# Optimization experiments

Hardware: AMD Instinct MI355X
Metric: run time of the kernel (lower is better)

The kernel has to match this reference:

```python
import jax, jax.numpy as jnp
import numpy as np

H = 256          # h_dim
SEQ_LEN = 10     # max history length
B = 2048         # number of queries with non-empty history
N = 327680       # total flattened neighbors across all (query, timestep) segments
NUM_SEG = B * SEQ_LEN
NUM_ENT = 20000
NUM_REL = 200


def setup_inputs() -> dict:
    key = jax.random.key(0)
    ks = jax.random.split(key, 9)
    s = jax.random.randint(ks[0], (B,), 0, NUM_ENT)
    r = jax.random.randint(ks[1], (B,), 0, NUM_REL)
    nbr_ids = jax.random.randint(ks[2], (N,), 0, NUM_ENT)
    seg_ids = jnp.sort(jax.random.randint(ks[3], (N,), 0, NUM_SEG))
    ent_embeds = jax.random.normal(ks[4], (NUM_ENT, H), dtype=jnp.float32)
    rel_embeds = jax.random.normal(ks[5], (NUM_REL, H), dtype=jnp.float32)
    W_attn = jax.random.normal(ks[6], (3 * H, H), dtype=jnp.float32) * 0.05
    b_attn = jax.random.normal(ks[7], (H,), dtype=jnp.float32) * 0.05
    v_s = jax.random.normal(ks[8], (H, 1), dtype=jnp.float32) * 0.05
    return {"s": s, "r": r, "nbr_ids": nbr_ids, "seg_ids": seg_ids,
            "ent_embeds": ent_embeds, "rel_embeds": rel_embeds,
            "W_attn": W_attn, "b_attn": b_attn, "v_s": v_s}


def reference(s, r, nbr_ids, seg_ids, ent_embeds, rel_embeds, W_attn, b_attn, v_s):
    # Per-neighbor gathers. Each neighbor belongs to segment seg = q*SEQ_LEN + t.
    q = seg_ids // SEQ_LEN                              # query index per neighbor [N]
    em = ent_embeds[nbr_ids]                            # [N, H] neighbor embeddings
    s_emb = ent_embeds[s]                               # [B, H]
    r_emb = rel_embeds[r]                               # [B, H]
    ss = s_emb[q]                                       # [N, H]
    rr = r_emb[q]                                       # [N, H]
    # Score: tanh(Linear(3H -> H)) @ v_s  -> scalar per neighbor
    x = jnp.concatenate([em, ss, rr], axis=1)           # [N, 3H]
    scores = (jnp.tanh(x @ W_attn + b_attn) @ v_s)[:, 0]  # [N]
    # Segment softmax over neighbors within each (query, timestep) segment.
    m = jax.ops.segment_max(scores, seg_ids, num_segments=NUM_SEG)  # [S]
    e = jnp.exp(scores - m[seg_ids])                    # [N]
    denom = jax.ops.segment_sum(e, seg_ids, num_segments=NUM_SEG)   # [S]
    w = e / denom[seg_ids]                              # [N]
    # Weighted sum of neighbor embeddings per segment (scatter-reduce).
    agg = jax.ops.segment_sum(w[:, None] * em, seg_ids, num_segments=NUM_SEG)  # [S, H]
    counts = jax.ops.segment_sum(jnp.ones_like(scores), seg_ids, num_segments=NUM_SEG)
    mask = (counts > 0).astype(em.dtype).reshape(B, SEQ_LEN, 1)     # present timesteps
    agg = agg.reshape(B, SEQ_LEN, H)
    ss_t = jnp.broadcast_to(s_emb[:, None, :], (B, SEQ_LEN, H))
    rr_t = jnp.broadcast_to(r_emb[:, None, :], (B, SEQ_LEN, H))
    # Padded [B, SEQ_LEN, 3H] sequence tensor (rows for empty segments are zero,
    # matching the torch code's zero-initialized padded tensor). Dropout p=0.0.
    out = jnp.concatenate([agg, ss_t, rr_t], axis=2) * mask
    return out
```

## Files before the change

### kernel.cpp

```cpp
#include <hip/hip_runtime.h>
#include <hip/hip_bf16.h>

#define H 256
#define SEQ 10
#define C2LOG2E 2.8853900817779268f
#define LOG2E 1.4426950408889634f

typedef __attribute__((ext_vector_type(8))) short bf16x8;
typedef __attribute__((ext_vector_type(4))) float f32x4;

__device__ __forceinline__ unsigned short f2bf(float x) {
    union { float f; unsigned u; } v; v.f = x;
    unsigned r = v.u + 0x7fff + ((v.u >> 16) & 1);
    return (unsigned short)(r >> 16);
}
__device__ __forceinline__ float bf2f(unsigned short b) {
    union { unsigned u; float f; } v; v.u = ((unsigned)b) << 16;
    return v.f;
}
__device__ __forceinline__ float fexp2(float x) {
    return __builtin_amdgcn_exp2f(x);
}

__global__ void prep_kernel(const float* __restrict__ W,
                            unsigned short* __restrict__ Wt,
                            const int* __restrict__ seg_ids,
                            int* __restrict__ seg_start,
                            int nTr, int n, int num_seg) {
    if ((int)blockIdx.x < nTr) {
        __shared__ float tile[64][65];
        int tk = blockIdx.x % 12;
        int tn = blockIdx.x / 12;
        int t = threadIdx.x;
        int rr = t >> 2;
        int rc = (t & 3) * 16;
        const float* src = W + (size_t)(tk * 64 + rr) * H + tn * 64 + rc;
        float4 a = *reinterpret_cast<const float4*>(src);
        float4 b = *reinterpret_cast<const float4*>(src + 4);
        float4 c = *reinterpret_cast<const float4*>(src + 8);
        float4 d = *reinterpret_cast<const float4*>(src + 12);
        tile[rr][rc + 0] = a.x;  tile[rr][rc + 1] = a.y;
        tile[rr][rc + 2] = a.z;  tile[rr][rc + 3] = a.w;
        tile[rr][rc + 4] = b.x;  tile[rr][rc + 5] = b.y;
        tile[rr][rc + 6] = b.z;  tile[rr][rc + 7] = b.w;
        tile[rr][rc + 8] = c.x;  tile[rr][rc + 9] = c.y;
        tile[rr][rc + 10] = c.z; tile[rr][rc + 11] = c.w;
        tile[rr][rc + 12] = d.x; tile[rr][rc + 13] = d.y;
        tile[rr][rc + 14] = d.z; tile[rr][rc + 15] = d.w;
        __syncthreads();
        bf16x8 o0, o1;
#pragma unroll
        for (int j = 0; j < 8; j++) {
            o0[j] = (short)f2bf(C2LOG2E * tile[rc + j][rr]);
            o1[j] = (short)f2bf(C2LOG2E * tile[rc + 8 + j][rr]);
        }
        unsigned short* dst = Wt + (size_t)(tn * 64 + rr) * (3 * H) + tk * 64 + rc;
        *reinterpret_cast<bf16x8*>(dst) = o0;
        *reinterpret_cast<bf16x8*>(dst + 8) = o1;
    } else {
        int j = (blockIdx.x - nTr) * 256 + threadIdx.x;
        if (j >= n) return;
        int cur = seg_ids[j];
        int prev = (j == 0) ? -1 : seg_ids[j - 1];
        for (int s2 = prev + 1; s2 <= cur; s2++) seg_start[s2] = j;
        if (j == n - 1)
            for (int s2 = cur + 1; s2 <= num_seg; s2++) seg_start[s2] = n;
    }
}

__global__ void gemm_bf16_kernel(const float* __restrict__ entf,
                                 const int* __restrict__ sidx,
                                 const int* __restrict__ ridx,
                                 const float* __restrict__ rel,
                                 const unsigned short* __restrict__ Wt,
                                 const float* __restrict__ bias,
                                 unsigned short* __restrict__ comb,
                                 unsigned short* __restrict__ qpart,
                                 int nEntBlk, int M0, int M1) {
    __shared__ unsigned short As[64][40];
    bool isEnt = (int)blockIdx.x < nEntBlk;
    int m0 = (isEnt ? blockIdx.x : (blockIdx.x - nEntBlk)) * 64;
    int M = isEnt ? M0 : M1;
    int K = isEnt ? H : 2 * H;
    int k0 = isEnt ? 0 : H;
    int ldo = isEnt ? 512 : H;
    unsigned short* outp = isEnt ? comb : qpart;

    int t = threadIdx.x;
    int sr = t >> 2;
    int sc = (t & 3) * 8;
    int wave = t >> 6, lane = t & 63;
    int lr = lane & 15, lg = lane >> 4;

    f32x4 acc[4][4];
#pragma unroll
    for (int i = 0; i < 4; i++)
#pragma unroll
        for (int jn = 0; jn < 4; jn++) acc[i][jn] = (f32x4){0.f, 0.f, 0.f, 0.f};

    const unsigned short* bp[4];
#pragma unroll
    for (int bn = 0; bn < 4; bn++)
        bp[bn] = Wt + (size_t)(wave * 64 + bn * 16 + lr) * (3 * H) + k0 + lg * 8;

    for (int kk = 0; kk < K; kk += 32) {
        bf16x8 av = {};
        int gm = m0 + sr;
        if (gm < M) {
            const float* src;
            if (isEnt) {
                src = entf + (size_t)gm * H + kk + sc;
            } else {
                int k = kk + sc;
                src = (k < H) ? (entf + (size_t)sidx[gm] * H + k)
                              : (rel + (size_t)ridx[gm] * H + (k - H));
            }
            float4 f0 = *reinterpret_cast<const float4*>(src);
            float4 f1 = *reinterpret_cast<const float4*>(src + 4);
            av[0] = (short)f2bf(f0.x); av[1] = (short)f2bf(f0.y);
            av[2] = (short)f2bf(f0.z); av[3] = (short)f2bf(f0.w);
            av[4] = (short)f2bf(f1.x); av[5] = (short)f2bf(f1.y);
            av[6] = (short)f2bf(f1.z); av[7] = (short)f2bf(f1.w);
            if (isEnt)
                *reinterpret_cast<bf16x8*>(comb + (size_t)gm * 512 + 256 + kk + sc) = av;
        }
        *reinterpret_cast<bf16x8*>(&As[sr][sc]) = av;

        bf16x8 bfr[4];
#pragma unroll
        for (int bn = 0; bn < 4; bn++)
            bfr[bn] = *reinterpret_cast<const bf16x8*>(bp[bn] + kk);

        __syncthreads();
        bf16x8 afr[4];
#pragma unroll
        for (int am = 0; am < 4; am++)
            afr[am] = *reinterpret_cast<const bf16x8*>(&As[am * 16 + lr][lg * 8]);
#pragma unroll
        for (int am = 0; am < 4; am++)
#pragma unroll
            for (int bn = 0; bn < 4; bn++)
                acc[am][bn] = __builtin_amdgcn_mfma_f32_16x16x32_bf16(
                    afr[am], bfr[bn], acc[am][bn], 0, 0, 0);
        __syncthreads();
    }

#pragma unroll
    for (int bn = 0; bn < 4; bn++) {
        int col = wave * 64 + bn * 16 + lr;
        float bv = isEnt ? 0.f : C2LOG2E * bias[col];
#pragma unroll
        for (int am = 0; am < 4; am++) {
#pragma unroll
            for (int rr = 0; rr < 4; rr++) {
                int row = m0 + am * 16 + lg * 4 + rr;
                if (row < M)
                    outp[(size_t)row * ldo + col] = f2bf(acc[am][bn][rr] + bv);
            }
        }
    }
}

__global__ void __launch_bounds__(128)
fused_agg_kernel(const int* __restrict__ nbr_ids,
                 const int* __restrict__ seg_start,
                 const unsigned short* __restrict__ comb,
                 const unsigned short* __restrict__ qpartbf,
                 const float* __restrict__ v_s,
                 const float* __restrict__ ent_embeds,
                 const float* __restrict__ rel_embeds,
                 const int* __restrict__ s,
                 const int* __restrict__ r,
                 float* __restrict__ out, int num_seg) {
    int seg = blockIdx.x * 2 + (threadIdx.x >> 6);
    if (seg >= num_seg) return;
    int lane = threadIdx.x & 63;
    int g = lane >> 4, li = lane & 15;
    int cb = li * 16;
    int c4 = lane * 4;
    int b = seg / SEQ;
    int start = seg_start[seg], end = seg_start[seg + 1];
    float* orow = out + (size_t)seg * (3 * H);

    if (start == end) {
        float4 z = {0.f, 0.f, 0.f, 0.f};
        *reinterpret_cast<float4*>(orow + c4) = z;
        *reinterpret_cast<float4*>(orow + H + c4) = z;
        *reinterpret_cast<float4*>(orow + 2 * H + c4) = z;
        return;
    }

    float4 ssv = *reinterpret_cast<const float4*>(ent_embeds + (size_t)s[b] * H + c4);
    float4 rrv = *reinterpret_cast<const float4*>(rel_embeds + (size_t)r[b] * H + c4);

    float vm2[16];
    float vsum = 0.f;
    {
        const float4* vp = reinterpret_cast<const float4*>(v_s + cb);
#pragma unroll
        for (int k = 0; k < 4; k++) {
            float4 tv = vp[k];
            vm2[4 * k + 0] = -2.f * tv.x; vm2[4 * k + 1] = -2.f * tv.y;
            vm2[4 * k + 2] = -2.f * tv.z; vm2[4 * k + 3] = -2.f * tv.w;
            vsum += tv.x + tv.y + tv.z + tv.w;
        }
    }

    float qv[16];
    {
        bf16x8 qa = *reinterpret_cast<const bf16x8*>(qpartbf + (size_t)b * H + cb);
        bf16x8 qb = *reinterpret_cast<const bf16x8*>(qpartbf + (size_t)b * H + cb + 8);
#pragma unroll
        for (int k = 0; k < 8; k++) {
            qv[k] = bf2f((unsigned short)qa[k]);
            qv[8 + k] = bf2f((unsigned short)qb[k]);
        }
    }

    float acc[16];
#pragma unroll
    for (int k = 0; k < 16; k++) acc[k] = 0.f;
    float lpart = 0.f;

    int cc = end - start;
    int nitm = (cc + 3) >> 2;

    bf16x8 p0 = {}, p1 = {}, e0 = {}, e1 = {};
    if (g < cc) {
        const unsigned short* row = comb + (size_t)nbr_ids[start + g] * 512 + cb;
        p0 = *reinterpret_cast<const bf16x8*>(row);
        p1 = *reinterpret_cast<const bf16x8*>(row + 8);
        e0 = *reinterpret_cast<const bf16x8*>(row + 256);
        e1 = *reinterpret_cast<const bf16x8*>(row + 264);
    }

    for (int ji = 0; ji < nitm; ji++) {
        bf16x8 p0n = {}, p1n = {}, e0n = {}, e1n = {};
        int jn = 4 * (ji + 1) + g;
        if (jn < cc) {
            const unsigned short* rown = comb + (size_t)nbr_ids[start + jn] * 512 + cb;
            p0n = *reinterpret_cast<const bf16x8*>(rown);
            p1n = *reinterpret_cast<const bf16x8*>(rown + 8);
            e0n = *reinterpret_cast<const bf16x8*>(rown + 256);
            e1n = *reinterpret_cast<const bf16x8*>(rown + 264);
        }

        float sa = 0.f, sb = 0.f;
#pragma unroll
        for (int k = 0; k < 8; k += 2) {
            float a0 = fexp2(bf2f((unsigned short)p0[k]) + qv[k]) + 1.f;
            float a1 = fexp2(bf2f((unsigned short)p1[k]) + qv[8 + k]) + 1.f;
            float num = vm2[k] * a1;
            num = fmaf(vm2[8 + k], a0, num);
            sa = fmaf(num, __builtin_amdgcn_rcpf(a0 * a1), sa);
            float b0 = fexp2(bf2f((unsigned short)p0[k + 1]) + qv[k + 1]) + 1.f;
            float b1 = fexp2(bf2f((unsigned short)p1[k + 1]) + qv[9 + k]) + 1.f;
            float numb = vm2[k + 1] * b1;
            numb = fmaf(vm2[9 + k], b0, numb);
            sb = fmaf(numb, __builtin_amdgcn_rcpf(b0 * b1), sb);
        }
        float s16 = sa + sb + vsum;
        s16 += __shfl_xor(s16, 1);
        s16 += __shfl_xor(s16, 2);
        s16 += __shfl_xor(s16, 4);
        s16 += __shfl_xor(s16, 8);
        float e = fexp2(s16 * LOG2E);
        e = (4 * ji + g < cc) ? e : 0.f;
        lpart += e;
#pragma unroll
        for (int k = 0; k < 8; k++) {
            acc[k] = fmaf(e, bf2f((unsigned short)e0[k]), acc[k]);
            acc[8 + k] = fmaf(e, bf2f((unsigned short)e1[k]), acc[8 + k]);
        }
        p0 = p0n; p1 = p1n; e0 = e0n; e1 = e1n;
    }

    lpart += __shfl_xor(lpart, 16);
    lpart += __shfl_xor(lpart, 32);
#pragma unroll
    for (int k = 0; k < 16; k++) {
        acc[k] += __shfl_xor(acc[k], 16);
        acc[k] += __shfl_xor(acc[k], 32);
    }
    float invl = 1.f / lpart;

    float4 o;
#pragma unroll
    for (int k = 0; k < 4; k++) {
        float v0 = acc[k], v1 = acc[4 + k], v2 = acc[8 + k], v3 = acc[12 + k];
        float pick = (g == 0) ? v0 : (g == 1) ? v1 : (g == 2) ? v2 : v3;
        if (k == 0) o.x = pick * invl;
        else if (k == 1) o.y = pick * invl;
        else if (k == 2) o.z = pick * invl;
        else o.w = pick * invl;
    }
    *reinterpret_cast<float4*>(orow + cb + 4 * g) = o;
    *reinterpret_cast<float4*>(orow + H + c4) = ssv;
    *reinterpret_cast<float4*>(orow + 2 * H + c4) = rrv;
}

extern "C" void kernel_launch(void* const* d_in, const int* in_sizes, int n_in,
                              void* d_out, int out_size, void* d_ws, size_t ws_size,
                              hipStream_t stream) {
    const int* s = (const int*)d_in[0];
    const int* r = (const int*)d_in[1];
    const int* nbr_ids = (const int*)d_in[2];
    const int* seg_ids = (const int*)d_in[3];
    const float* ent_embeds = (const float*)d_in[4];
    const float* rel_embeds = (const float*)d_in[5];
    const float* W_attn = (const float*)d_in[6];
    const float* b_attn = (const float*)d_in[7];
    const float* v_s = (const float*)d_in[8];
    float* out = (float*)d_out;

    int B = in_sizes[0];
    int N = in_sizes[2];
    int num_ent = in_sizes[4] / H;
    int num_seg = B * SEQ;

    char* ws = (char*)d_ws;
    unsigned short* comb = (unsigned short*)ws;
    unsigned short* Wt = comb + (size_t)num_ent * 512;
    unsigned short* qpartbf = Wt + (size_t)H * 3 * H;
    int* seg_start = (int*)(qpartbf + (size_t)B * H);

    int nTr = 12 * 4;
    int nSeg = (N + 255) / 256;
    prep_kernel<<<nTr + nSeg, 256, 0, stream>>>(W_attn, Wt, seg_ids, seg_start,
                                                nTr, N, num_seg);

    int nEntBlk = (num_ent + 63) / 64;
    int nQBlk = B / 64;
    gemm_bf16_kernel<<<nEntBlk + nQBlk, 256, 0, stream>>>(
        ent_embeds, s, r, rel_embeds, Wt, b_attn, comb, qpartbf,
        nEntBlk, num_ent, B);

    fused_agg_kernel<<<(num_seg + 1) / 2, 128, 0, stream>>>(
        nbr_ids, seg_start, comb, qpartbf, v_s,
        ent_embeds, rel_embeds, s, r, out, num_seg);
}
```

Before: 91.11 us.

## Shrink GEMM row tile to 32, deepen K step, move segment-start build into GEMM launch

The GEMM block now covers 32 rows instead of 64 and steps K by 64 instead of 32. This doubles the block count for better CU occupancy on the 20000-entity GEMM and halves the number of barrier iterations. The seg_start construction moves out of the W-transpose prep kernel into extra blocks of the GEMM launch, leaving prep as a tiny 48-block kernel. Each B-fragment load is now reused across only two A sub-tiles instead of four, which raises global/L2 traffic on the weight matrix.

```diff
diff --git a/kernel.cpp b/kernel.cpp
--- a/kernel.cpp
+++ b/kernel.cpp
@@ -23,49 +23,36 @@
 }
 
 __global__ void prep_kernel(const float* __restrict__ W,
-                            unsigned short* __restrict__ Wt,
-                            const int* __restrict__ seg_ids,
-                            int* __restrict__ seg_start,
-                            int nTr, int n, int num_seg) {
-    if ((int)blockIdx.x < nTr) {
-        __shared__ float tile[64][65];
-        int tk = blockIdx.x % 12;
-        int tn = blockIdx.x / 12;
-        int t = threadIdx.x;
-        int rr = t >> 2;
-        int rc = (t & 3) * 16;
-        const float* src = W + (size_t)(tk * 64 + rr) * H + tn * 64 + rc;
-        float4 a = *reinterpret_cast<const float4*>(src);
-        float4 b = *reinterpret_cast<const float4*>(src + 4);
-        float4 c = *reinterpret_cast<const float4*>(src + 8);
-        float4 d = *reinterpret_cast<const float4*>(src + 12);
-        tile[rr][rc + 0] = a.x;  tile[rr][rc + 1] = a.y;
-        tile[rr][rc + 2] = a.z;  tile[rr][rc + 3] = a.w;
-        tile[rr][rc + 4] = b.x;  tile[rr][rc + 5] = b.y;
-        tile[rr][rc + 6] = b.z;  tile[rr][rc + 7] = b.w;
-        tile[rr][rc + 8] = c.x;  tile[rr][rc + 9] = c.y;
-        tile[rr][rc + 10] = c.z; tile[rr][rc + 11] = c.w;
-        tile[rr][rc + 12] = d.x; tile[rr][rc + 13] = d.y;
-        tile[rr][rc + 14] = d.z; tile[rr][rc + 15] = d.w;
-        __syncthreads();
-        bf16x8 o0, o1;
-#pragma unroll
-        for (int j = 0; j < 8; j++) {
-            o0[j] = (short)f2bf(C2LOG2E * tile[rc + j][rr]);
-            o1[j] = (short)f2bf(C2LOG2E * tile[rc + 8 + j][rr]);
-        }
-        unsigned short* dst = Wt + (size_t)(tn * 64 + rr) * (3 * H) + tk * 64 + rc;
-        *reinterpret_cast<bf16x8*>(dst) = o0;
-        *reinterpret_cast<bf16x8*>(dst + 8) = o1;
-    } else {
-        int j = (blockIdx.x - nTr) * 256 + threadIdx.x;
-        if (j >= n) return;
-        int cur = seg_ids[j];
-        int prev = (j == 0) ? -1 : seg_ids[j - 1];
-        for (int s2 = prev + 1; s2 <= cur; s2++) seg_start[s2] = j;
-        if (j == n - 1)
-            for (int s2 = cur + 1; s2 <= num_seg; s2++) seg_start[s2] = n;
-    }
+                            unsigned short* __restrict__ Wt) {
+    __shared__ float tile[64][65];
+    int tk = blockIdx.x % 12;
+    int tn = blockIdx.x / 12;
+    int t = threadIdx.x;
+    int rr = t >> 2;
+    int rc = (t & 3) * 16;
+    const float* src = W + (size_t)(tk * 64 + rr) * H + tn * 64 + rc;
+    float4 a = *reinterpret_cast<const float4*>(src);
+    float4 b = *reinterpret_cast<const float4*>(src + 4);
+    float4 c = *reinterpret_cast<const float4*>(src + 8);
+    float4 d = *reinterpret_cast<const float4*>(src + 12);
+    tile[rr][rc + 0] = a.x;  tile[rr][rc + 1] = a.y;
+    tile[rr][rc + 2] = a.z;  tile[rr][rc + 3] = a.w;
+    tile[rr][rc + 4] = b.x;  tile[rr][rc + 5] = b.y;
+    tile[rr][rc + 6] = b.z;  tile[rr][rc + 7] = b.w;
+    tile[rr][rc + 8] = c.x;  tile[rr][rc + 9] = c.y;
+    tile[rr][rc + 10] = c.z; tile[rr][rc + 11] = c.w;
+    tile[rr][rc + 12] = d.x; tile[rr][rc + 13] = d.y;
+    tile[rr][rc + 14] = d.z; tile[rr][rc + 15] = d.w;
+    __syncthreads();
+    bf16x8 o0, o1;
+#pragma unroll
+    for (int j = 0; j < 8; j++) {
+        o0[j] = (short)f2bf(C2LOG2E * tile[rc + j][rr]);
+        o1[j] = (short)f2bf(C2LOG2E * tile[rc + 8 + j][rr]);
+    }
+    unsigned short* dst = Wt + (size_t)(tn * 64 + rr) * (3 * H) + tk * 64 + rc;
+    *reinterpret_cast<bf16x8*>(dst) = o0;
+    *reinterpret_cast<bf16x8*>(dst + 8) = o1;
 }
 
 __global__ void gemm_bf16_kernel(const float* __restrict__ entf,
@@ -76,10 +63,25 @@
                                  const float* __restrict__ bias,
                                  unsigned short* __restrict__ comb,
                                  unsigned short* __restrict__ qpart,
-                                 int nEntBlk, int M0, int M1) {
-    __shared__ unsigned short As[64][40];
-    bool isEnt = (int)blockIdx.x < nEntBlk;
-    int m0 = (isEnt ? blockIdx.x : (blockIdx.x - nEntBlk)) * 64;
+                                 const int* __restrict__ seg_ids,
+                                 int* __restrict__ seg_start,
+                                 int n, int num_seg,
+                                 int nEntBlk, int nQBlk, int M0, int M1) {
+    __shared__ unsigned short As[32][72];
+    int bid = blockIdx.x;
+    if (bid >= nEntBlk + nQBlk) {
+        int j = (bid - nEntBlk - nQBlk) * 256 + threadIdx.x;
+        if (j >= n) return;
+        int cur = seg_ids[j];
+        int prev = (j == 0) ? -1 : seg_ids[j - 1];
+        for (int s2 = prev + 1; s2 <= cur; s2++) seg_start[s2] = j;
+        if (j == n - 1)
+            for (int s2 = cur + 1; s2 <= num_seg; s2++) seg_start[s2] = n;
+        return;
+    }
+
+    bool isEnt = bid < nEntBlk;
+    int m0 = (isEnt ? bid : (bid - nEntBlk)) * 32;
     int M = isEnt ? M0 : M1;
     int K = isEnt ? H : 2 * H;
     int k0 = isEnt ? 0 : H;
@@ -87,14 +89,14 @@
     unsigned short* outp = isEnt ? comb : qpart;
 
     int t = threadIdx.x;
-    int sr = t >> 2;
-    int sc = (t & 3) * 8;
+    int sr = t >> 3;
+    int sc = (t & 7) * 8;
     int wave = t >> 6, lane = t & 63;
     int lr = lane & 15, lg = lane >> 4;
 
-    f32x4 acc[4][4];
-#pragma unroll
-    for (int i = 0; i < 4; i++)
+    f32x4 acc[2][4];
+#pragma unroll
+    for (int i = 0; i < 2; i++)
 #pragma unroll
         for (int jn = 0; jn < 4; jn++) acc[i][jn] = (f32x4){0.f, 0.f, 0.f, 0.f};
 
@@ -103,7 +105,7 @@
     for (int bn = 0; bn < 4; bn++)
         bp[bn] = Wt + (size_t)(wave * 64 + bn * 16 + lr) * (3 * H) + k0 + lg * 8;
 
-    for (int kk = 0; kk < K; kk += 32) {
+    for (int kk = 0; kk < K; kk += 64) {
         bf16x8 av = {};
         int gm = m0 + sr;
         if (gm < M) {
@@ -126,22 +128,27 @@
         }
         *reinterpret_cast<bf16x8*>(&As[sr][sc]) = av;
 
-        bf16x8 bfr[4];
-#pragma unroll
-        for (int bn = 0; bn < 4; bn++)
-            bfr[bn] = *reinterpret_cast<const bf16x8*>(bp[bn] + kk);
+        bf16x8 bfr[2][4];
+#pragma unroll
+        for (int kh = 0; kh < 2; kh++)
+#pragma unroll
+            for (int bn = 0; bn < 4; bn++)
+                bfr[kh][bn] = *reinterpret_cast<const bf16x8*>(bp[bn] + kk + kh * 32);
 
         __syncthreads();
-        bf16x8 afr[4];
-#pragma unroll
-        for (int am = 0; am < 4; am++)
-            afr[am] = *reinterpret_cast<const bf16x8*>(&As[am * 16 + lr][lg * 8]);
-#pragma unroll
-        for (int am = 0; am < 4; am++)
-#pragma unroll
-            for (int bn = 0; bn < 4; bn++)
-                acc[am][bn] = __builtin_amdgcn_mfma_f32_16x16x32_bf16(
-                    afr[am], bfr[bn], acc[am][bn], 0, 0, 0);
+#pragma unroll
+        for (int kh = 0; kh < 2; kh++) {
+            bf16x8 afr[2];
+#pragma unroll
+            for (int am = 0; am < 2; am++)
+                afr[am] = *reinterpret_cast<const bf16x8*>(&As[am * 16 + lr][kh * 32 + lg * 8]);
+#pragma unroll
+            for (int am = 0; am < 2; am++)
+#pragma unroll
+                for (int bn = 0; bn < 4; bn++)
+                    acc[am][bn] = __builtin_amdgcn_mfma_f32_16x16x32_bf16(
+                        afr[am], bfr[kh][bn], acc[am][bn], 0, 0, 0);
+        }
         __syncthreads();
     }
 
@@ -150,7 +157,7 @@
         int col = wave * 64 + bn * 16 + lr;
         float bv = isEnt ? 0.f : C2LOG2E * bias[col];
 #pragma unroll
-        for (int am = 0; am < 4; am++) {
+        for (int am = 0; am < 2; am++) {
 #pragma unroll
             for (int rr = 0; rr < 4; rr++) {
                 int row = m0 + am * 16 + lg * 4 + rr;
@@ -324,16 +331,14 @@
     unsigned short* qpartbf = Wt + (size_t)H * 3 * H;
     int* seg_start = (int*)(qpartbf + (size_t)B * H);
 
-    int nTr = 12 * 4;
-    int nSeg = (N + 255) / 256;
-    prep_kernel<<<nTr + nSeg, 256, 0, stream>>>(W_attn, Wt, seg_ids, seg_start,
-                                                nTr, N, num_seg);
-
-    int nEntBlk = (num_ent + 63) / 64;
-    int nQBlk = B / 64;
-    gemm_bf16_kernel<<<nEntBlk + nQBlk, 256, 0, stream>>>(
+    prep_kernel<<<48, 256, 0, stream>>>(W_attn, Wt);
+
+    int nEntBlk = (num_ent + 31) / 32;
+    int nQBlk = B / 32;
+    int nSegBlk = (N + 255) / 256;
+    gemm_bf16_kernel<<<nEntBlk + nQBlk + nSegBlk, 256, 0, stream>>>(
         ent_embeds, s, r, rel_embeds, Wt, b_attn, comb, qpartbf,
-        nEntBlk, num_ent, B);
+        seg_ids, seg_start, N, num_seg, nEntBlk, nQBlk, num_ent, B);
 
     fused_agg_kernel<<<(num_seg + 1) / 2, 128, 0, stream>>>(
         nbr_ids, seg_start, comb, qpartbf, v_s,
```

Result: faster. 89.07 us (median of 2 runs) (-2.2%).
